# Performance work log

Measured on AMD Instinct MI355X. Metric: run time of the kernel, lower is better.

The kernel has to match this reference:

```python
import jax, jax.numpy as jnp
import numpy as np

TEMP = 0.02
KD_W = 1.0
VSD_W = 1.0
VLAD_W = 1.0
CON_W = 1.0
MSE_W = 1.0

B, SS, ST, DS, DT, V, NV, NT = 8, 96, 128, 1024, 2048, 32000, 32, 64


def hungarian(cost):
    # Shortest-augmenting-path assignment (e-maxx / Jonker-Volgenant style).
    # Square cost [n, n]; returns col_of_row so that row i matches column
    # col_of_row[i] with minimal total cost (same as scipy linear_sum_assignment).
    cost = np.asarray(cost, dtype=np.float64)
    n = cost.shape[0]
    INF = 1e18
    u = np.zeros(n + 1)
    v = np.zeros(n + 1)
    p = np.zeros(n + 1, dtype=np.int64)
    way = np.zeros(n + 1, dtype=np.int64)
    for i in range(1, n + 1):
        p[0] = i
        j0 = 0
        minv = np.full(n + 1, INF)
        used = np.zeros(n + 1, dtype=bool)
        while True:
            used[j0] = True
            i0 = p[j0]
            js = np.nonzero(~used)[0]
            js = js[js > 0]
            cur = cost[i0 - 1, js - 1] - u[i0] - v[js]
            upd = cur < minv[js]
            minv[js] = np.where(upd, cur, minv[js])
            way[js] = np.where(upd, j0, way[js])
            k = int(np.argmin(minv[js]))
            delta = minv[js][k]
            j1 = int(js[k])
            u[p[used]] += delta
            v[used] -= delta
            minv[~used] -= delta
            j0 = j1
            if p[j0] == 0:
                break
        while j0:
            j1 = int(way[j0])
            p[j0] = p[j1]
            j0 = j1
    col_of_row = np.zeros(n, dtype=np.int64)
    for j in range(1, n + 1):
        col_of_row[p[j] - 1] = j - 1
    return col_of_row


def _match(s_logits, t_logits):
    # Per-sample L1 (p=1 cdist) cost between teacher rows and student cols,
    # then Hungarian matching. Host-side loop is unavoidable (sequential
    # combinatorial algorithm), matching the original per-sample scipy loop.
    idx = []
    for b in range(s_logits.shape[0]):
        cost = np.abs(t_logits[b][:, None, :] - s_logits[b][None, :, :]).sum(-1)
        idx.append(hungarian(cost))
    return np.stack(idx)


def _cosine(a, b, eps=1e-8):
    # a: [B, M, D], b: [B, N, D] -> [B, M, N]; torch F.cosine_similarity semantics
    an = a / jnp.maximum(jnp.linalg.norm(a, axis=-1, keepdims=True), eps)
    bn = b / jnp.maximum(jnp.linalg.norm(b, axis=-1, keepdims=True), eps)
    return jnp.einsum('bmd,bnd->bmn', an, bn)


def setup_inputs() -> dict:
    key = jax.random.key(0)
    ks = jax.random.split(key, 12)
    f = jax.random.normal
    return {
        's_qry_reps': f(ks[0], (B, DS), jnp.float32),
        's_pos_reps': f(ks[1], (B, DS), jnp.float32),
        't_qry_reps': f(ks[2], (B, DT), jnp.float32),
        't_pos_reps': f(ks[3], (B, DT), jnp.float32),
        's_hidden_qry': f(ks[4], (B, SS, DS), jnp.float32),
        's_hidden_pos': f(ks[5], (B, SS, DS), jnp.float32),
        't_hidden_qry': f(ks[6], (B, ST, DT), jnp.float32),
        't_hidden_pos': f(ks[7], (B, ST, DT), jnp.float32),
        'W_s_lm': f(ks[8], (DS, V), jnp.float32) / np.float32(np.sqrt(DS)),
        'W_t_lm': f(ks[9], (DT, V), jnp.float32) / np.float32(np.sqrt(DT)),
        'W_proj': f(ks[10], (DT, DS), jnp.float32) / np.float32(np.sqrt(DT)),
        'b_proj': jnp.zeros((DS,), jnp.float32),
        'nv': NV,
        'nt': NT,
    }


def reference(s_qry_reps, s_pos_reps, t_qry_reps, t_pos_reps,
              s_hidden_qry, s_hidden_pos, t_hidden_qry, t_hidden_pos,
              W_s_lm, W_t_lm, W_proj, b_proj, nv, nt):
    Bn = s_qry_reps.shape[0]
    # 1) contrastive InfoNCE (world_size=1 -> gather is identity, target=arange)
    scores = (s_qry_reps @ s_pos_reps.T) / TEMP
    logp = jax.nn.log_softmax(scores, axis=-1)
    contrastive = -jnp.mean(jnp.diagonal(logp))
    # 2) MSE vs t2s-projected teacher reps
    mse = 0.5 * (jnp.mean((s_qry_reps - (t_qry_reps @ W_proj + b_proj)) ** 2)
                 + jnp.mean((s_pos_reps - (t_pos_reps @ W_proj + b_proj)) ** 2))
    # 3/4) VSD + VLAD over qry and pos sides stacked -> [2B, ...]
    s_hid = jnp.concatenate([s_hidden_qry, s_hidden_pos], axis=0)
    t_hid = jnp.concatenate([t_hidden_qry, t_hidden_pos], axis=0)
    St = t_hid.shape[1]
    sv = s_hid[:, :nv]                      # student vision tokens   [2B, Nv, DS]
    st = s_hid[:, nv:nv + nt]               # student text tokens     [2B, Nt, DS]
    tv = t_hid[:, St - nv - nt:St - nt]     # teacher vision tokens   [2B, Nv, DT]
    tt = t_hid[:, St - nt:]                 # teacher text tokens     [2B, Nt, DT]
    s_logits = jnp.einsum('bnd,dv->bnv', sv, W_s_lm)   # [2B, Nv, V]
    t_logits = jnp.einsum('bnd,dv->bnv', tv, W_t_lm)   # [2B, Nv, V]
    # Hungarian matching on detached logits (host side, like the original)
    idx = jnp.asarray(_match(np.asarray(s_logits), np.asarray(t_logits)))  # [2B, Nv]
    # VSD: MSE between matched student logits and teacher logits (t order = arange)
    s_logits_m = jnp.take_along_axis(s_logits, idx[:, :, None], axis=1)
    vsd = jnp.sum(jnp.mean((s_logits_m - t_logits) ** 2, axis=(1, 2)))
    # VLAD: smooth-L1 on vision->text cosine affinity maps
    sv_m = jnp.take_along_axis(sv, idx[:, :, None], axis=1)
    d = _cosine(sv_m, st) - _cosine(tv, tt)            # [2B, Nv, Nt]
    ad = jnp.abs(d)
    sl1 = jnp.where(ad < 1.0, 0.5 * d * d, ad - 0.5)
    vlad = jnp.sum(jnp.mean(sl1, axis=(1, 2)))
    distill = (VSD_W * vsd + VLAD_W * vlad) / Bn
    loss = CON_W * contrastive + MSE_W * mse + KD_W * distill
    return loss, contrastive, distill
```

## Files before the change

### kernel.cpp

```cpp
#include <hip/hip_runtime.h>
#include <math.h>

#define DS_ 1024
#define DT_ 2048
#define V_  32000
#define SS_ 96
#define ST_ 128


__device__ __forceinline__ float block_reduce_sum_256(float v) {
  __shared__ float tmp[4];
  #pragma unroll
  for (int off = 32; off; off >>= 1) v += __shfl_xor(v, off);
  const int wid = threadIdx.x >> 6;
  if ((threadIdx.x & 63) == 0) tmp[wid] = v;
  __syncthreads();
  if (threadIdx.x == 0) v = tmp[0] + tmp[1] + tmp[2] + tmp[3];
  return v;
}

__device__ __forceinline__ const float* s_base(int b, const float* s_hq, const float* s_hp) {
  return (b < 8) ? (s_hq + (size_t)b * SS_ * DS_) : (s_hp + (size_t)(b - 8) * SS_ * DS_);
}
__device__ __forceinline__ const float* t_base(int b, const float* t_hq, const float* t_hp) {
  return (b < 8) ? (t_hq + (size_t)b * ST_ * DT_) : (t_hp + (size_t)(b - 8) * ST_ * DT_);
}

__device__ __forceinline__ unsigned short f2bf(float x) {
  unsigned int u = __float_as_uint(x);
  u += 0x7fffu + ((u >> 16) & 1u);
  return (unsigned short)(u >> 16);
}
__device__ __forceinline__ float bf2f(unsigned short u) {
  return __uint_as_float(((unsigned int)u) << 16);
}

using bf16x8 = __attribute__((ext_vector_type(8))) short;
using f32x4  = __attribute__((ext_vector_type(4))) float;
using u16x4  = __attribute__((ext_vector_type(4))) unsigned short;

__device__ __forceinline__ void gll16(const void* g, void* l) {
  __builtin_amdgcn_global_load_lds((const __attribute__((address_space(1))) unsigned int*)g,
                                   (__attribute__((address_space(3))) unsigned int*)l, 16, 0, 0);
}

__device__ __forceinline__ unsigned int wave_umin_dpp(unsigned int r) {
  unsigned int t;
  t = (unsigned int)__builtin_amdgcn_update_dpp((int)r, (int)r, 0x111, 0xF, 0xF, false); r = r < t ? r : t;
  t = (unsigned int)__builtin_amdgcn_update_dpp((int)r, (int)r, 0x112, 0xF, 0xF, false); r = r < t ? r : t;
  t = (unsigned int)__builtin_amdgcn_update_dpp((int)r, (int)r, 0x114, 0xF, 0xF, false); r = r < t ? r : t;
  t = (unsigned int)__builtin_amdgcn_update_dpp((int)r, (int)r, 0x118, 0xF, 0xF, false); r = r < t ? r : t;
  t = (unsigned int)__builtin_amdgcn_update_dpp((int)r, (int)r, 0x142, 0xF, 0xF, false); r = r < t ? r : t;
  t = (unsigned int)__builtin_amdgcn_update_dpp((int)r, (int)r, 0x143, 0xF, 0xF, false); r = r < t ? r : t;
  return r;
}


__device__ __forceinline__ void scores_body(int blk, const float* __restrict__ sq,
                                            const float* __restrict__ sp,
                                            float* __restrict__ scores) {
  const int i = blk >> 3, j = blk & 7;
  float acc = 0.f;
  for (int k = threadIdx.x; k < DS_; k += 256)
    acc += sq[(size_t)i * DS_ + k] * sp[(size_t)j * DS_ + k];
  acc = block_reduce_sum_256(acc);
  if (threadIdx.x == 0) scores[i * 8 + j] = acc * 50.0f;
}

__device__ __forceinline__ void proj2_body(int kc, const float* __restrict__ t_qry,
                                           const float* __restrict__ t_pos,
                                           const float* __restrict__ Wp,
                                           float* __restrict__ proj,
                                           unsigned char* smem) {
  float (*tv)[64] = (float (*)[64])smem;
  const int tid = threadIdx.x;
  for (int s = tid; s < 16 * 64; s += 256) {
    const int zi = s >> 6, k = s & 63;
    const float* t = (zi >= 8) ? (t_pos + (size_t)(zi - 8) * DT_) : (t_qry + (size_t)zi * DT_);
    tv[zi][k] = t[kc * 64 + k];
  }
  __syncthreads();
  const int d4 = tid * 4;
  float4 acc[16];
  #pragma unroll
  for (int zi = 0; zi < 16; ++zi) acc[zi] = (float4){0.f, 0.f, 0.f, 0.f};
  for (int k = 0; k < 64; ++k) {
    const float4 w = *(const float4*)&Wp[(size_t)(kc * 64 + k) * DS_ + d4];
    #pragma unroll
    for (int zi = 0; zi < 16; ++zi) {
      const float t = tv[zi][k];
      acc[zi].x += t * w.x; acc[zi].y += t * w.y;
      acc[zi].z += t * w.z; acc[zi].w += t * w.w;
    }
  }
  #pragma unroll
  for (int zi = 0; zi < 16; ++zi) {
    float* p = proj + (size_t)zi * DS_ + d4;
    atomicAdd(&p[0], acc[zi].x); atomicAdd(&p[1], acc[zi].y);
    atomicAdd(&p[2], acc[zi].z); atomicAdd(&p[3], acc[zi].w);
  }
}

__device__ __forceinline__ void norms_body(int blk, const float* __restrict__ s_hq,
                                           const float* __restrict__ s_hp,
                                           const float* __restrict__ t_hq,
                                           const float* __restrict__ t_hp,
                                           float* __restrict__ invn) {
  const int b = blk / 192, t = blk % 192;
  const float* bs = s_base(b, s_hq, s_hp);
  const float* bt = t_base(b, t_hq, t_hp);
  const float* row;
  int K;
  float* out;
  if (t < 32)       { row = bs + (size_t)t * DS_;             K = DS_; out = invn + b * 32 + t; }
  else if (t < 96)  { row = bs + (size_t)t * DS_;             K = DS_; out = invn + 512 + b * 64 + (t - 32); }
  else if (t < 128) { row = bt + (size_t)(t - 96 + 32) * DT_;  K = DT_; out = invn + 1536 + b * 32 + (t - 96); }
  else              { row = bt + (size_t)(t - 128 + 64) * DT_; K = DT_; out = invn + 2048 + b * 64 + (t - 128); }
  float ss = 0.f;
  for (int k = threadIdx.x; k < K; k += 256) { const float x = row[k]; ss += x * x; }
  ss = block_reduce_sum_256(ss);
  if (threadIdx.x == 0) *out = 1.0f / fmaxf(sqrtf(ss), 1e-8f);
}

__device__ __forceinline__ void pack_as_body(int g, const float* __restrict__ s_hq,
                                             const float* __restrict__ s_hp,
                                             unsigned short* __restrict__ As) {
  const int b = g >> 5, i = g & 31;
  const float* src = s_base(b, s_hq, s_hp) + (size_t)i * DS_;
  const int k4 = threadIdx.x * 4;
  const float4 w = *(const float4*)&src[k4];
  u16x4 o; o[0] = f2bf(w.x); o[1] = f2bf(w.y); o[2] = f2bf(w.z); o[3] = f2bf(w.w);
  *(u16x4*)&As[(size_t)g * DS_ + k4] = o;
}

__device__ __forceinline__ void pack_at_body(int g, const float* __restrict__ t_hq,
                                             const float* __restrict__ t_hp,
                                             unsigned short* __restrict__ At) {
  const int b = g >> 5, i = g & 31;
  const float* src = t_base(b, t_hq, t_hp) + (size_t)(32 + i) * DT_;
  #pragma unroll
  for (int it = 0; it < 2; ++it) {
    const int k4 = (threadIdx.x + it * 256) * 4;
    const float4 w = *(const float4*)&src[k4];
    u16x4 o; o[0] = f2bf(w.x); o[1] = f2bf(w.y); o[2] = f2bf(w.z); o[3] = f2bf(w.w);
    *(u16x4*)&At[(size_t)g * DT_ + k4] = o;
  }
}

__device__ __forceinline__ void convw_body(int id, const float* __restrict__ W,
                                           unsigned short* __restrict__ Wbt,
                                           int K, unsigned char* smem) {
  float (*tile)[65] = (float (*)[65])smem;
  const int v0 = (id % 500) * 64, k0 = (id / 500) * 64;
  const int tid = threadIdx.x;
  #pragma unroll
  for (int it = 0; it < 4; ++it) {
    const int kr = (tid >> 4) + it * 16;
    const int v4 = (tid & 15) * 4;
    const float4 w = *(const float4*)&W[(size_t)(k0 + kr) * V_ + v0 + v4];
    tile[v4 + 0][kr] = w.x; tile[v4 + 1][kr] = w.y;
    tile[v4 + 2][kr] = w.z; tile[v4 + 3][kr] = w.w;
  }
  __syncthreads();
  #pragma unroll
  for (int it = 0; it < 2; ++it) {
    const int s = tid + it * 256;
    const int v = s >> 3, ch = s & 7;
    const float* src = &tile[v][ch * 8];
    unsigned int o[4];
    #pragma unroll
    for (int q = 0; q < 4; ++q)
      o[q] = (unsigned int)f2bf(src[2 * q]) | ((unsigned int)f2bf(src[2 * q + 1]) << 16);
    uint4 pk = {o[0], o[1], o[2], o[3]};
    *(uint4*)&Wbt[(size_t)(v0 + v) * K + k0 + ch * 8] = pk;
  }
}

__device__ __forceinline__ void dt_body(int id, const float* __restrict__ t_hq,
                                        const float* __restrict__ t_hp,
                                        const float* __restrict__ invn,
                                        float* __restrict__ ct) {
  const int b = id >> 5, i = id & 31;
  const int wv = threadIdx.x >> 6, lane = threadIdx.x & 63;
  const float* bt = t_base(b, t_hq, t_hp);
  const float* a2p = bt + (size_t)(32 + i) * DT_;
  float a2[32];
  #pragma unroll
  for (int q = 0; q < 32; ++q) a2[q] = a2p[lane + 64 * q];
  const float in_t = invn[1536 + b * 32 + i];
  for (int jj = 0; jj < 16; ++jj) {
    const int j = wv * 16 + jj;
    const float* b2 = bt + (size_t)(64 + j) * DT_;
    float dt = 0.f;
    #pragma unroll
    for (int q = 0; q < 32; ++q) dt += a2[q] * b2[lane + 64 * q];
    #pragma unroll
    for (int off = 32; off; off >>= 1) dt += __shfl_xor(dt, off);
    if (lane == 0) ct[(b * 32 + i) * 64 + j] = dt * in_t * invn[2048 + b * 64 + j];
  }
}


template <int K>
__device__ __forceinline__ void gemm_body(int blk, int nwg,
                                          const unsigned short* __restrict__ A,
                                          const unsigned short* __restrict__ Wbt,
                                          unsigned short* __restrict__ Out,
                                          unsigned char* smem) {
  unsigned short* AldsB = (unsigned short*)smem;
  unsigned short* BldsB = (unsigned short*)(smem + 32768);
  const int q = nwg >> 3, r = nwg & 7;
  const int xcd = blk & 7, off = blk >> 3;
  const int sblk = (xcd < r ? xcd * (q + 1) : r * (q + 1) + (xcd - r) * q) + off;
  const int m0 = (sblk & 1) * 256;
  const int n0 = (sblk >> 1) * 128;
  const int tid = threadIdx.x;
  const int wv = tid >> 6, lane = tid & 63;
  const int lr = lane & 15, cc = lane >> 4;

  f32x4 acc[4][8];
  #pragma unroll
  for (int mf = 0; mf < 4; ++mf)
    #pragma unroll
    for (int nf = 0; nf < 8; ++nf) acc[mf][nf] = (f32x4){0.f, 0.f, 0.f, 0.f};

  constexpr int NT = K / 32;

  auto stage = [&](int kt, int buf) {
    #pragma unroll
    for (int it = 0; it < 4; ++it) {
      const int slot = it * 256 + tid;
      const int row = slot >> 2, cs = slot & 3;
      gll16(A + (size_t)(m0 + row) * K + kt * 32 + ((cs ^ ((row >> 1) & 3)) << 3),
            AldsB + (size_t)buf * 8192 + (size_t)(it * 256 + wv * 64) * 8);
    }
    #pragma unroll
    for (int it = 0; it < 2; ++it) {
      const int slot = it * 256 + tid;
      const int row = slot >> 2, cs = slot & 3;
      gll16(Wbt + (size_t)(n0 + row) * K + kt * 32 + ((cs ^ ((row >> 1) & 3)) << 3),
            BldsB + (size_t)buf * 4096 + (size_t)(it * 256 + wv * 64) * 8);
    }
  };

  stage(0, 0);
  if (NT > 1) stage(1, 1);
  for (int kt = 0; kt < NT; ++kt) {
    const int cur = kt & 1;
    if (kt >= 1 && kt + 1 < NT) stage(kt + 1, cur ^ 1);
    if (kt + 1 < NT) asm volatile("s_waitcnt vmcnt(6)" ::: "memory");
    else             asm volatile("s_waitcnt vmcnt(0)" ::: "memory");
    asm volatile("s_barrier" ::: "memory");
    bf16x8 af[4];
    #pragma unroll
    for (int mf = 0; mf < 4; ++mf) {
      const int row = wv * 64 + mf * 16 + lr;
      af[mf] = *(const bf16x8*)(AldsB + cur * 8192 + row * 32 + ((cc ^ ((row >> 1) & 3)) << 3));
    }
    __builtin_amdgcn_s_setprio(1);
    #pragma unroll
    for (int nf = 0; nf < 8; ++nf) {
      const int vr = nf * 16 + lr;
      const bf16x8 bfr = *(const bf16x8*)(BldsB + cur * 4096 + vr * 32 + ((cc ^ ((vr >> 1) & 3)) << 3));
      #pragma unroll
      for (int mf = 0; mf < 4; ++mf)
        acc[mf][nf] = __builtin_amdgcn_mfma_f32_16x16x32_bf16(af[mf], bfr, acc[mf][nf], 0, 0, 0);
    }
    __builtin_amdgcn_s_setprio(0);
    asm volatile("s_barrier" ::: "memory");
  }

  unsigned short* Olds = AldsB;
  #pragma unroll
  for (int h = 0; h < 2; ++h) {
    if (h) __syncthreads();
    #pragma unroll
    for (int mf = 0; mf < 4; ++mf)
      #pragma unroll
      for (int nf4 = 0; nf4 < 4; ++nf4) {
        const int nf = h * 4 + nf4;
        #pragma unroll
        for (int q2 = 0; q2 < 4; ++q2) {
          const int row = wv * 64 + mf * 16 + (lane >> 4) * 4 + q2;
          const int col = nf4 * 16 + lr;
          Olds[row * 64 + (col ^ (((row >> 2) & 3) << 4))] = f2bf(acc[mf][nf][q2]);
        }
      }
    __syncthreads();
    #pragma unroll
    for (int it = 0; it < 4; ++it) {
      const int slot = it * 256 + tid;
      const int row = slot >> 3, c2 = slot & 7;
      const uint4 pk = *(const uint4*)&Olds[row * 64 + ((c2 ^ (((row >> 2) & 3) << 1)) << 3)];
      *(uint4*)&Out[(size_t)(m0 + row) * V_ + n0 + h * 64 + c2 * 8] = pk;
    }
  }
}


__global__ __launch_bounds__(256) void fused_pre_kernel(const float* __restrict__ s_qry,
                                                        const float* __restrict__ s_pos,
                                                        const float* __restrict__ t_qry,
                                                        const float* __restrict__ t_pos,
                                                        const float* __restrict__ s_hq,
                                                        const float* __restrict__ s_hp,
                                                        const float* __restrict__ t_hq,
                                                        const float* __restrict__ t_hp,
                                                        const float* __restrict__ Ws,
                                                        const float* __restrict__ Wp,
                                                        float* __restrict__ scores,
                                                        float* __restrict__ proj,
                                                        float* __restrict__ invn,
                                                        unsigned short* __restrict__ As,
                                                        unsigned short* __restrict__ At,
                                                        unsigned short* __restrict__ Wsb) {
  __shared__ __align__(16) unsigned char smem[16640];
  const int blk = blockIdx.x;
  if (blk < 64)            scores_body(blk, s_qry, s_pos, scores);
  else if (blk < 96)       proj2_body(blk - 64, t_qry, t_pos, Wp, proj, smem);
  else if (blk < 3168)     norms_body(blk - 96, s_hq, s_hp, t_hq, t_hp, invn);
  else if (blk < 3680)     pack_as_body(blk - 3168, s_hq, s_hp, As);
  else if (blk < 4192)     pack_at_body(blk - 3680, t_hq, t_hp, At);
  else                     convw_body(blk - 4192, Ws, Wsb, DS_, smem);
}

__global__ __launch_bounds__(256) void fused_mid_kernel(const unsigned short* __restrict__ As,
                                                        const unsigned short* __restrict__ Wsb,
                                                        unsigned short* __restrict__ Sg,
                                                        const float* __restrict__ Wt,
                                                        unsigned short* __restrict__ Wtb,
                                                        const float* __restrict__ t_hq,
                                                        const float* __restrict__ t_hp,
                                                        const float* __restrict__ invn,
                                                        float* __restrict__ ct) {
  __shared__ __align__(16) unsigned char smem[49152];
  const int blk = blockIdx.x;
  if (blk < 500)            gemm_body<DS_>(blk, 500, As, Wsb, Sg, smem);
  else if (blk < 16500)     convw_body(blk - 500, Wt, Wtb, DT_, smem);
  else                      dt_body(blk - 16500, t_hq, t_hp, invn, ct);
}

__global__ __launch_bounds__(256) void gemm_tn_kernel_t(const unsigned short* __restrict__ A,
                                                        const unsigned short* __restrict__ Wbt,
                                                        unsigned short* __restrict__ Out) {
  __shared__ __align__(16) unsigned char smem[49152];
  gemm_body<DT_>(blockIdx.x, (int)gridDim.x, A, Wbt, Out, smem);
}


__global__ __launch_bounds__(256) void mse2_kernel(const float* __restrict__ s_qry,
                                                   const float* __restrict__ s_pos,
                                                   const float* __restrict__ proj,
                                                   const float* __restrict__ bp,
                                                   float* __restrict__ mse_acc) {
  const int z = blockIdx.x >> 3, i = blockIdx.x & 7;
  const float* s = (z ? s_pos : s_qry) + (size_t)i * DS_;
  const float* p = proj + ((size_t)z * 8 + i) * DS_;
  float ss = 0.f;
  for (int d = threadIdx.x; d < DS_; d += 256) {
    const float diff = s[d] - (p[d] + bp[d]);
    ss += diff * diff;
  }
  ss = block_reduce_sum_256(ss);
  if (threadIdx.x == 0) atomicAdd(mse_acc, ss);
}


#define CPV 500
#define CPP 508

__global__ __launch_bounds__(256) void cost_pairs_kernel(const unsigned short* __restrict__ Sg,
                                                         const unsigned short* __restrict__ Tg,
                                                         float* __restrict__ cost1,
                                                         float* __restrict__ cost2) {
  __shared__ __align__(16) unsigned short Sl[32 * CPP];
  __shared__ __align__(16) unsigned short Tl[32 * CPP];
  const int b = blockIdx.x >> 6, sl = blockIdx.x & 63;
  const int v0 = sl * CPV;
  const int tid = threadIdx.x;

  for (int s = tid; s < 32 * 125; s += 256) {
    const int r = s / 125, c = s % 125;
    *(u16x4*)&Sl[r * CPP + c * 4] = *(const u16x4*)&Sg[(size_t)(b * 32 + r) * V_ + v0 + c * 4];
    *(u16x4*)&Tl[r * CPP + c * 4] = *(const u16x4*)&Tg[(size_t)(b * 32 + r) * V_ + v0 + c * 4];
  }
  __syncthreads();

  const int i = tid >> 3, j4 = (tid & 7) * 4;
  float a1[4] = {0.f, 0.f, 0.f, 0.f}, a2[4] = {0.f, 0.f, 0.f, 0.f};
  for (int v = 0; v < CPV; v += 4) {
    const u16x4 t4 = *(const u16x4*)&Tl[i * CPP + v];
    float tf[4];
    #pragma unroll
    for (int q = 0; q < 4; ++q) tf[q] = bf2f(t4[q]);
    #pragma unroll
    for (int jj = 0; jj < 4; ++jj) {
      const u16x4 s4 = *(const u16x4*)&Sl[(j4 + jj) * CPP + v];
      #pragma unroll
      for (int q = 0; q < 4; ++q) {
        const float d = tf[q] - bf2f(s4[q]);
        a1[jj] += fabsf(d);
        a2[jj] += d * d;
      }
    }
  }
  #pragma unroll
  for (int jj = 0; jj < 4; ++jj) {
    atomicAdd(&cost1[(size_t)b * 1024 + i * 32 + j4 + jj], a1[jj]);
    atomicAdd(&cost2[(size_t)b * 1024 + i * 32 + j4 + jj], a2[jj]);
  }
}


__global__ __launch_bounds__(64) void hungarian_kernel(const float* __restrict__ cost1,
                                                       const float* __restrict__ cost2,
                                                       int* __restrict__ idx,
                                                       float* __restrict__ vsd_acc) {
  const int b = blockIdx.x;
  const int lane = threadIdx.x;
  const float INF = __int_as_float(0x7f800000);
  __shared__ float C[32 * 33];
  __shared__ float u_lds[33];

  for (int s = lane; s < 1024; s += 64) {
    const int r = s >> 5, c = s & 31;
    C[r * 33 + c] = cost1[(size_t)b * 1024 + s];
  }
  if (lane == 0) u_lds[0] = 0.f;
  __syncthreads();

  const bool isj = (lane >= 1 && lane <= 32);
  const int cix = isj ? (lane - 1) : 0;

  if (lane < 32) {
    float m = C[lane * 33];
    for (int j = 1; j < 32; ++j) m = fminf(m, C[lane * 33 + j]);
    u_lds[lane + 1] = m;
  }
  __syncthreads();

  float v = 0.f;
  if (isj) {
    float m = INF;
    for (int i = 0; i < 32; ++i) m = fminf(m, C[i * 33 + cix] - u_lds[i + 1]);
    v = m;
  }

  int p = 0;
  unsigned int assigned = 0;
  for (int i = 1; i <= 32; ++i) {
    const float ui = u_lds[i];
    const bool zero = isj && (p == 0) && ((C[(i - 1) * 33 + cix] - ui) == v);
    const unsigned long long tie = __ballot(zero);
    if (tie) {
      const int j1 = __ffsll(tie) - 1;
      if (lane == j1) p = i;
      assigned |= (1u << (i - 1));
    }
  }

  for (int i = 1; i <= 32; ++i) {
    if (assigned & (1u << (i - 1))) continue;
    if (lane == 0) p = i;
    float minv = INF;
    int way = 0;
    int used = 0;
    int j0 = 0;
    float ui0 = u_lds[i];
    float crow = C[(i - 1) * 33 + cix];
    while (true) {
      if (lane == j0) used = 1;
      float val = INF;
      if (isj && !used) {
        const float cur = crow - ui0 - v;
        if (cur < minv) { minv = cur; way = j0; }
        val = minv;
      }
      const unsigned int rb = wave_umin_dpp(__float_as_uint(val));
      const unsigned int minb = (unsigned int)__builtin_amdgcn_readlane((int)rb, 63);
      const float delta = __uint_as_float(minb);
      const unsigned long long tie = __ballot(__float_as_uint(val) == minb);
      const int j1 = __ffsll(tie) - 1;
      const int i0n = __builtin_amdgcn_readlane(p, j1);
      const float ui0n = u_lds[i0n];
      const int nri = (i0n >= 1 ? i0n : 1) - 1;
      const float cnext = C[nri * 33 + cix];
      if (used) {
        u_lds[p] += delta;
        v -= delta;
      } else {
        minv -= delta;
      }
      j0 = j1;
      if (i0n == 0) break;
      ui0 = ui0n;
      crow = cnext;
    }
    while (j0) {
      const int j1 = __builtin_amdgcn_readlane(way, j0);
      const int pv = __builtin_amdgcn_readlane(p, j1);
      if (lane == j0) p = pv;
      j0 = j1;
    }
  }
  float term = 0.f;
  if (isj) {
    idx[b * 32 + (p - 1)] = lane - 1;
    term = cost2[(size_t)b * 1024 + (p - 1) * 32 + (lane - 1)];
  }
  #pragma unroll
  for (int off = 32; off; off >>= 1) term += __shfl_xor(term, off);
  if (lane == 0) atomicAdd(vsd_acc, term);
}


__global__ __launch_bounds__(256) void vlad_final_kernel(const float* __restrict__ s_hq,
                                                         const float* __restrict__ s_hp,
                                                         const int* __restrict__ idx,
                                                         const float* __restrict__ invn,
                                                         const float* __restrict__ ct,
                                                         float* __restrict__ vlad_acc) {
  const int b = blockIdx.x >> 5, i = blockIdx.x & 31;
  const int wv = threadIdx.x >> 6, lane = threadIdx.x & 63;
  const float* bs = s_base(b, s_hq, s_hp);
  const int is = idx[b * 32 + i];
  const float* a1p = bs + (size_t)is * DS_;
  float a1[16];
  #pragma unroll
  for (int q = 0; q < 16; ++q) a1[q] = a1p[lane + 64 * q];
  const float in_s = invn[b * 32 + is];
  float local = 0.f;
  for (int jj = 0; jj < 16; ++jj) {
    const int j = wv * 16 + jj;
    const float* b1 = bs + (size_t)(32 + j) * DS_;
    float ds = 0.f;
    #pragma unroll
    for (int q = 0; q < 16; ++q) ds += a1[q] * b1[lane + 64 * q];
    #pragma unroll
    for (int off = 32; off; off >>= 1) ds += __shfl_xor(ds, off);
    if (lane == 0) {
      const float cs = ds * in_s * invn[512 + b * 64 + j];
      const float d = cs - ct[(b * 32 + i) * 64 + j];
      const float ad = fabsf(d);
      local += (ad < 1.f) ? 0.5f * d * d : ad - 0.5f;
    }
  }
  if (lane == 0) atomicAdd(vlad_acc, local);
}


__global__ __launch_bounds__(64) void final_kernel(const float* __restrict__ scores,
                                                   const float* __restrict__ accs,
                                                   float* __restrict__ out) {
  const int lane = threadIdx.x;
  float ci = 0.f;
  if (lane < 8) {
    float m = -1e30f;
    for (int j = 0; j < 8; ++j) m = fmaxf(m, scores[lane * 8 + j]);
    float sum = 0.f;
    for (int j = 0; j < 8; ++j) sum += expf(scores[lane * 8 + j] - m);
    const float lse = m + logf(sum);
    ci = scores[lane * 8 + lane] - lse;
  }
  #pragma unroll
  for (int off = 32; off; off >>= 1) ci += __shfl_xor(ci, off);
  if (lane == 0) {
    const float contrastive = -ci / 8.0f;
    const float mse = accs[0] / 16384.0f;
    const float vsd = accs[1] / 1024000.0f;
    const float vlad = accs[2] / 2048.0f;
    const float distill = (vsd + vlad) / 8.0f;
    out[0] = contrastive + mse + distill;
    out[1] = contrastive;
    out[2] = distill;
  }
}


extern "C" void kernel_launch(void* const* d_in, const int* in_sizes, int n_in,
                              void* d_out, int out_size, void* d_ws, size_t ws_size,
                              hipStream_t stream) {
  const float* s_qry = (const float*)d_in[0];
  const float* s_pos = (const float*)d_in[1];
  const float* t_qry = (const float*)d_in[2];
  const float* t_pos = (const float*)d_in[3];
  const float* s_hq  = (const float*)d_in[4];
  const float* s_hp  = (const float*)d_in[5];
  const float* t_hq  = (const float*)d_in[6];
  const float* t_hp  = (const float*)d_in[7];
  const float* Ws    = (const float*)d_in[8];
  const float* Wt    = (const float*)d_in[9];
  const float* Wp    = (const float*)d_in[10];
  const float* bp    = (const float*)d_in[11];

  float* ws     = (float*)d_ws;
  float* scores = ws;
  float* cost1  = ws + 64;
  float* cost2  = ws + 16448;
  float* invn   = ws + 32832;
  float* accs   = ws + 35904;
  float* proj   = ws + 35908;
  int*   idx    = (int*)(ws + 52292);
  float* ct     = ws + 52804;
  const size_t small_bytes = (size_t)52804 * 4;

  const size_t As_off = 524288;
  const size_t At_off = As_off + (size_t)512 * DS_ * 2;
  const size_t Ws_off = At_off + (size_t)512 * DT_ * 2;
  const size_t Wt_off = Ws_off + (size_t)V_ * DS_ * 2;
  const size_t Sg_off = Wt_off + (size_t)V_ * DT_ * 2;
  const size_t Tg_off = Sg_off + (size_t)512 * V_ * 2;
  const size_t req2   = Tg_off + (size_t)512 * V_ * 2;

  hipMemsetAsync(d_ws, 0, small_bytes, stream);

  if (ws_size >= req2) {
    unsigned short* As  = (unsigned short*)((char*)d_ws + As_off);
    unsigned short* At  = (unsigned short*)((char*)d_ws + At_off);
    unsigned short* Wsb = (unsigned short*)((char*)d_ws + Ws_off);
    unsigned short* Wtb = (unsigned short*)((char*)d_ws + Wt_off);
    unsigned short* Sg  = (unsigned short*)((char*)d_ws + Sg_off);
    unsigned short* Tg  = (unsigned short*)((char*)d_ws + Tg_off);

    fused_pre_kernel<<<12192, 256, 0, stream>>>(s_qry, s_pos, t_qry, t_pos,
                                                s_hq, s_hp, t_hq, t_hp,
                                                Ws, Wp, scores, proj, invn, As, At, Wsb);
    mse2_kernel<<<16, 256, 0, stream>>>(s_qry, s_pos, proj, bp, accs + 0);

    fused_mid_kernel<<<17012, 256, 0, stream>>>(As, Wsb, Sg, Wt, Wtb,
                                                t_hq, t_hp, invn, ct);

    gemm_tn_kernel_t<<<(V_ / 128) * 2, 256, 0, stream>>>(At, Wtb, Tg);
    cost_pairs_kernel<<<16 * 64, 256, 0, stream>>>(Sg, Tg, cost1, cost2);

    hungarian_kernel<<<16, 64, 0, stream>>>(cost1, cost2, idx, accs + 1);
    vlad_final_kernel<<<512, 256, 0, stream>>>(s_hq, s_hp, idx, invn, ct, accs + 2);
    final_kernel<<<1, 64, 0, stream>>>(scores, accs, (float*)d_out);
  }
}
```

Before: 463.8 us.

## Fuse teacher GEMM with cost computation and precompute VLAD cosine tables

The teacher logits GEMM now computes the L1/L2 pairwise cost directly from its accumulator tile against student logits staged in shared memory. This removes the Tg round trip to global memory and the separate cost_pairs kernel. All student and teacher vision-text dot products are precomputed in the pre kernel, so the post-Hungarian VLAD step becomes a small gather. The mse2 kernel is folded into the mid kernel, which removes launches. In exchange, the GEMM epilogue carries heavy register arrays and many atomics, and the cost loop repeats LDS reads per thread.

```diff
diff --git a/kernel.cpp b/kernel.cpp
--- a/kernel.cpp
+++ b/kernel.cpp
@@ -38,6 +38,7 @@
 using bf16x8 = __attribute__((ext_vector_type(8))) short;
 using f32x4  = __attribute__((ext_vector_type(4))) float;
 using u16x4  = __attribute__((ext_vector_type(4))) unsigned short;
+using u16x8  = __attribute__((ext_vector_type(8))) unsigned short;
 
 __device__ __forceinline__ void gll16(const void* g, void* l) {
   __builtin_amdgcn_global_load_lds((const __attribute__((address_space(1))) unsigned int*)g,
@@ -178,8 +179,7 @@
 
 __device__ __forceinline__ void dt_body(int id, const float* __restrict__ t_hq,
                                         const float* __restrict__ t_hp,
-                                        const float* __restrict__ invn,
-                                        float* __restrict__ ct) {
+                                        float* __restrict__ dtd) {
   const int b = id >> 5, i = id & 31;
   const int wv = threadIdx.x >> 6, lane = threadIdx.x & 63;
   const float* bt = t_base(b, t_hq, t_hp);
@@ -187,7 +187,6 @@
   float a2[32];
   #pragma unroll
   for (int q = 0; q < 32; ++q) a2[q] = a2p[lane + 64 * q];
-  const float in_t = invn[1536 + b * 32 + i];
   for (int jj = 0; jj < 16; ++jj) {
     const int j = wv * 16 + jj;
     const float* b2 = bt + (size_t)(64 + j) * DT_;
@@ -196,33 +195,60 @@
     for (int q = 0; q < 32; ++q) dt += a2[q] * b2[lane + 64 * q];
     #pragma unroll
     for (int off = 32; off; off >>= 1) dt += __shfl_xor(dt, off);
-    if (lane == 0) ct[(b * 32 + i) * 64 + j] = dt * in_t * invn[2048 + b * 64 + j];
-  }
+    if (lane == 0) dtd[(b * 32 + i) * 64 + j] = dt;
+  }
+}
+
+__device__ __forceinline__ void cs_body(int id, const float* __restrict__ s_hq,
+                                        const float* __restrict__ s_hp,
+                                        float* __restrict__ csd) {
+  const int b = id >> 5, i = id & 31;
+  const int wv = threadIdx.x >> 6, lane = threadIdx.x & 63;
+  const float* bs = s_base(b, s_hq, s_hp);
+  const float* a1p = bs + (size_t)i * DS_;
+  float a1[16];
+  #pragma unroll
+  for (int q = 0; q < 16; ++q) a1[q] = a1p[lane + 64 * q];
+  for (int jj = 0; jj < 16; ++jj) {
+    const int j = wv * 16 + jj;
+    const float* b1 = bs + (size_t)(32 + j) * DS_;
+    float ds = 0.f;
+    #pragma unroll
+    for (int q = 0; q < 16; ++q) ds += a1[q] * b1[lane + 64 * q];
+    #pragma unroll
+    for (int off = 32; off; off >>= 1) ds += __shfl_xor(ds, off);
+    if (lane == 0) csd[(b * 32 + i) * 64 + j] = ds;
+  }
+}
+
+__device__ __forceinline__ void mse2_body(int blk, const float* __restrict__ s_qry,
+                                          const float* __restrict__ s_pos,
+                                          const float* __restrict__ proj,
+                                          const float* __restrict__ bp,
+                                          float* __restrict__ mse_acc) {
+  const int z = blk >> 3, i = blk & 7;
+  const float* s = (z ? s_pos : s_qry) + (size_t)i * DS_;
+  const float* p = proj + ((size_t)z * 8 + i) * DS_;
+  float ss = 0.f;
+  for (int d = threadIdx.x; d < DS_; d += 256) {
+    const float diff = s[d] - (p[d] + bp[d]);
+    ss += diff * diff;
+  }
+  ss = block_reduce_sum_256(ss);
+  if (threadIdx.x == 0) atomicAdd(mse_acc, ss);
 }
 
 
 template <int K>
-__device__ __forceinline__ void gemm_body(int blk, int nwg,
-                                          const unsigned short* __restrict__ A,
-                                          const unsigned short* __restrict__ Wbt,
-                                          unsigned short* __restrict__ Out,
-                                          unsigned char* smem) {
+__device__ __forceinline__ void gemm_mainloop(int m0, int n0,
+                                              const unsigned short* __restrict__ A,
+                                              const unsigned short* __restrict__ Wbt,
+                                              f32x4 (&acc)[4][8], unsigned char* smem) {
   unsigned short* AldsB = (unsigned short*)smem;
   unsigned short* BldsB = (unsigned short*)(smem + 32768);
-  const int q = nwg >> 3, r = nwg & 7;
-  const int xcd = blk & 7, off = blk >> 3;
-  const int sblk = (xcd < r ? xcd * (q + 1) : r * (q + 1) + (xcd - r) * q) + off;
-  const int m0 = (sblk & 1) * 256;
-  const int n0 = (sblk >> 1) * 128;
   const int tid = threadIdx.x;
   const int wv = tid >> 6, lane = tid & 63;
   const int lr = lane & 15, cc = lane >> 4;
-
-  f32x4 acc[4][8];
-  #pragma unroll
-  for (int mf = 0; mf < 4; ++mf)
-    #pragma unroll
-    for (int nf = 0; nf < 8; ++nf) acc[mf][nf] = (f32x4){0.f, 0.f, 0.f, 0.f};
 
   constexpr int NT = K / 32;
 
@@ -269,8 +295,31 @@
     __builtin_amdgcn_s_setprio(0);
     asm volatile("s_barrier" ::: "memory");
   }
-
-  unsigned short* Olds = AldsB;
+}
+
+__device__ __forceinline__ void gemm_store_body(int blk, int nwg,
+                                                const unsigned short* __restrict__ A,
+                                                const unsigned short* __restrict__ Wbt,
+                                                unsigned short* __restrict__ Out,
+                                                unsigned char* smem) {
+  const int q = nwg >> 3, r = nwg & 7;
+  const int xcd = blk & 7, off = blk >> 3;
+  const int sblk = (xcd < r ? xcd * (q + 1) : r * (q + 1) + (xcd - r) * q) + off;
+  const int m0 = (sblk & 1) * 256;
+  const int n0 = (sblk >> 1) * 128;
+  const int tid = threadIdx.x;
+  const int wv = tid >> 6, lane = tid & 63;
+  const int lr = lane & 15;
+
+  f32x4 acc[4][8];
+  #pragma unroll
+  for (int mf = 0; mf < 4; ++mf)
+    #pragma unroll
+    for (int nf = 0; nf < 8; ++nf) acc[mf][nf] = (f32x4){0.f, 0.f, 0.f, 0.f};
+
+  gemm_mainloop<DS_>(m0, n0, A, Wbt, acc, smem);
+
+  unsigned short* Olds = (unsigned short*)smem;
   #pragma unroll
   for (int h = 0; h < 2; ++h) {
     if (h) __syncthreads();
@@ -294,6 +343,90 @@
       const uint4 pk = *(const uint4*)&Olds[row * 64 + ((c2 ^ (((row >> 2) & 3) << 1)) << 3)];
       *(uint4*)&Out[(size_t)(m0 + row) * V_ + n0 + h * 64 + c2 * 8] = pk;
     }
+  }
+}
+
+__global__ __launch_bounds__(256) void gemm_cost_kernel(const unsigned short* __restrict__ A,
+                                                        const unsigned short* __restrict__ Wbt,
+                                                        const unsigned short* __restrict__ Sg,
+                                                        float* __restrict__ cost1,
+                                                        float* __restrict__ cost2) {
+  __shared__ __align__(16) unsigned char smem[51200];
+  const int nwg = (int)gridDim.x;
+  const int q = nwg >> 3, r = nwg & 7;
+  const int xcd = blockIdx.x & 7, off = blockIdx.x >> 3;
+  const int sblk = (xcd < r ? xcd * (q + 1) : r * (q + 1) + (xcd - r) * q) + off;
+  const int m0 = (sblk & 1) * 256;
+  const int n0 = (sblk >> 1) * 128;
+  const int tid = threadIdx.x;
+  const int wv = tid >> 6, lane = tid & 63;
+  const int lr = lane & 15;
+
+  f32x4 acc[4][8];
+  #pragma unroll
+  for (int mf = 0; mf < 4; ++mf)
+    #pragma unroll
+    for (int nf = 0; nf < 8; ++nf) acc[mf][nf] = (f32x4){0.f, 0.f, 0.f, 0.f};
+
+  gemm_mainloop<DT_>(m0, n0, A, Wbt, acc, smem);
+
+  unsigned short* Tl   = (unsigned short*)smem;
+  unsigned short* Slds = (unsigned short*)(smem + 34816);
+  const int b8 = tid >> 5;
+  const int i  = tid & 31;
+  float l1[32], l2[32];
+  #pragma unroll
+  for (int j = 0; j < 32; ++j) { l1[j] = 0.f; l2[j] = 0.f; }
+
+  #pragma unroll
+  for (int h = 0; h < 2; ++h) {
+    if (h) __syncthreads();
+    #pragma unroll
+    for (int mf = 0; mf < 4; ++mf)
+      #pragma unroll
+      for (int nf4 = 0; nf4 < 4; ++nf4) {
+        #pragma unroll
+        for (int q2 = 0; q2 < 4; ++q2) {
+          const int row = wv * 64 + mf * 16 + (lane >> 4) * 4 + q2;
+          const int col = nf4 * 16 + lr;
+          Tl[row * 68 + col] = f2bf(acc[mf][h * 4 + nf4][q2]);
+        }
+      }
+    #pragma unroll
+    for (int qq = 0; qq < 2; ++qq) {
+      __syncthreads();
+      const int vbase = n0 + h * 64 + qq * 32;
+      #pragma unroll
+      for (int it = 0; it < 4; ++it) {
+        const int slot = it * 256 + tid;
+        const int srow = slot >> 2, c16 = slot & 3;
+        *(u16x8*)&Slds[srow * 32 + c16 * 8] =
+            *(const u16x8*)&Sg[(size_t)(m0 + srow) * V_ + vbase + c16 * 8];
+      }
+      __syncthreads();
+      for (int vq = 0; vq < 8; ++vq) {
+        const u16x4 t4 = *(const u16x4*)&Tl[tid * 68 + qq * 32 + vq * 4];
+        float tf[4];
+        #pragma unroll
+        for (int e = 0; e < 4; ++e) tf[e] = bf2f(t4[e]);
+        #pragma unroll
+        for (int j = 0; j < 32; ++j) {
+          const u16x4 s4 = *(const u16x4*)&Slds[(b8 * 32 + j) * 32 + vq * 4];
+          #pragma unroll
+          for (int e = 0; e < 4; ++e) {
+            const float d = tf[e] - bf2f(s4[e]);
+            l1[j] += fabsf(d);
+            l2[j] += d * d;
+          }
+        }
+      }
+    }
+  }
+  const int bglob = (m0 >> 5) + b8;
+  #pragma unroll
+  for (int j = 0; j < 32; ++j) {
+    atomicAdd(&cost1[(size_t)bglob * 1024 + i * 32 + j], l1[j]);
+    atomicAdd(&cost2[(size_t)bglob * 1024 + i * 32 + j], l2[j]);
   }
 }
 
@@ -313,7 +446,9 @@
                                                         float* __restrict__ invn,
                                                         unsigned short* __restrict__ As,
                                                         unsigned short* __restrict__ At,
-                                                        unsigned short* __restrict__ Wsb) {
+                                                        unsigned short* __restrict__ Wsb,
+                                                        float* __restrict__ csd,
+                                                        float* __restrict__ dtd) {
   __shared__ __align__(16) unsigned char smem[16640];
   const int blk = blockIdx.x;
   if (blk < 64)            scores_body(blk, s_qry, s_pos, scores);
@@ -321,7 +456,9 @@
   else if (blk < 3168)     norms_body(blk - 96, s_hq, s_hp, t_hq, t_hp, invn);
   else if (blk < 3680)     pack_as_body(blk - 3168, s_hq, s_hp, As);
   else if (blk < 4192)     pack_at_body(blk - 3680, t_hq, t_hp, At);
-  else                     convw_body(blk - 4192, Ws, Wsb, DS_, smem);
+  else if (blk < 12192)    convw_body(blk - 4192, Ws, Wsb, DS_, smem);
+  else if (blk < 12704)    cs_body(blk - 12192, s_hq, s_hp, csd);
+  else                     dt_body(blk - 12704, t_hq, t_hp, dtd);
 }
 
 __global__ __launch_bounds__(256) void fused_mid_kernel(const unsigned short* __restrict__ As,
@@ -329,86 +466,16 @@
                                                         unsigned short* __restrict__ Sg,
                                                         const float* __restrict__ Wt,
                                                         unsigned short* __restrict__ Wtb,
-                                                        const float* __restrict__ t_hq,
-                                                        const float* __restrict__ t_hp,
-                                                        const float* __restrict__ invn,
-                                                        float* __restrict__ ct) {
+                                                        const float* __restrict__ s_qry,
+                                                        const float* __restrict__ s_pos,
+                                                        const float* __restrict__ proj,
+                                                        const float* __restrict__ bp,
+                                                        float* __restrict__ mse_acc) {
   __shared__ __align__(16) unsigned char smem[49152];
   const int blk = blockIdx.x;
-  if (blk < 500)            gemm_body<DS_>(blk, 500, As, Wsb, Sg, smem);
+  if (blk < 500)            gemm_store_body(blk, 500, As, Wsb, Sg, smem);
   else if (blk < 16500)     convw_body(blk - 500, Wt, Wtb, DT_, smem);
-  else                      dt_body(blk - 16500, t_hq, t_hp, invn, ct);
-}
-
-__global__ __launch_bounds__(256) void gemm_tn_kernel_t(const unsigned short* __restrict__ A,
-                                                        const unsigned short* __restrict__ Wbt,
-                                                        unsigned short* __restrict__ Out) {
-  __shared__ __align__(16) unsigned char smem[49152];
-  gemm_body<DT_>(blockIdx.x, (int)gridDim.x, A, Wbt, Out, smem);
-}
-
-
-__global__ __launch_bounds__(256) void mse2_kernel(const float* __restrict__ s_qry,
-                                                   const float* __restrict__ s_pos,
-                                                   const float* __restrict__ proj,
-                                                   const float* __restrict__ bp,
-                                                   float* __restrict__ mse_acc) {
-  const int z = blockIdx.x >> 3, i = blockIdx.x & 7;
-  const float* s = (z ? s_pos : s_qry) + (size_t)i * DS_;
-  const float* p = proj + ((size_t)z * 8 + i) * DS_;
-  float ss = 0.f;
-  for (int d = threadIdx.x; d < DS_; d += 256) {
-    const float diff = s[d] - (p[d] + bp[d]);
-    ss += diff * diff;
-  }
-  ss = block_reduce_sum_256(ss);
-  if (threadIdx.x == 0) atomicAdd(mse_acc, ss);
-}
-
-
-#define CPV 500
-#define CPP 508
-
-__global__ __launch_bounds__(256) void cost_pairs_kernel(const unsigned short* __restrict__ Sg,
-                                                         const unsigned short* __restrict__ Tg,
-                                                         float* __restrict__ cost1,
-                                                         float* __restrict__ cost2) {
-  __shared__ __align__(16) unsigned short Sl[32 * CPP];
-  __shared__ __align__(16) unsigned short Tl[32 * CPP];
-  const int b = blockIdx.x >> 6, sl = blockIdx.x & 63;
-  const int v0 = sl * CPV;
-  const int tid = threadIdx.x;
-
-  for (int s = tid; s < 32 * 125; s += 256) {
-    const int r = s / 125, c = s % 125;
-    *(u16x4*)&Sl[r * CPP + c * 4] = *(const u16x4*)&Sg[(size_t)(b * 32 + r) * V_ + v0 + c * 4];
-    *(u16x4*)&Tl[r * CPP + c * 4] = *(const u16x4*)&Tg[(size_t)(b * 32 + r) * V_ + v0 + c * 4];
-  }
-  __syncthreads();
-
-  const int i = tid >> 3, j4 = (tid & 7) * 4;
-  float a1[4] = {0.f, 0.f, 0.f, 0.f}, a2[4] = {0.f, 0.f, 0.f, 0.f};
-  for (int v = 0; v < CPV; v += 4) {
-    const u16x4 t4 = *(const u16x4*)&Tl[i * CPP + v];
-    float tf[4];
-    #pragma unroll
-    for (int q = 0; q < 4; ++q) tf[q] = bf2f(t4[q]);
-    #pragma unroll
-    for (int jj = 0; jj < 4; ++jj) {
-      const u16x4 s4 = *(const u16x4*)&Sl[(j4 + jj) * CPP + v];
-      #pragma unroll
-      for (int q = 0; q < 4; ++q) {
-        const float d = tf[q] - bf2f(s4[q]);
-        a1[jj] += fabsf(d);
-        a2[jj] += d * d;
-      }
-    }
-  }
-  #pragma unroll
-  for (int jj = 0; jj < 4; ++jj) {
-    atomicAdd(&cost1[(size_t)b * 1024 + i * 32 + j4 + jj], a1[jj]);
-    atomicAdd(&cost2[(size_t)b * 1024 + i * 32 + j4 + jj], a2[jj]);
-  }
+  else                      mse2_body(blk - 16500, s_qry, s_pos, proj, bp, mse_acc);
 }
 
 
@@ -514,38 +581,26 @@
 }
 
 
-__global__ __launch_bounds__(256) void vlad_final_kernel(const float* __restrict__ s_hq,
-                                                         const float* __restrict__ s_hp,
-                                                         const int* __restrict__ idx,
-                                                         const float* __restrict__ invn,
-                                                         const float* __restrict__ ct,
-                                                         float* __restrict__ vlad_acc) {
-  const int b = blockIdx.x >> 5, i = blockIdx.x & 31;
-  const int wv = threadIdx.x >> 6, lane = threadIdx.x & 63;
-  const float* bs = s_base(b, s_hq, s_hp);
-  const int is = idx[b * 32 + i];
-  const float* a1p = bs + (size_t)is * DS_;
-  float a1[16];
-  #pragma unroll
-  for (int q = 0; q < 16; ++q) a1[q] = a1p[lane + 64 * q];
-  const float in_s = invn[b * 32 + is];
+__global__ __launch_bounds__(256) void vlad_gather_kernel(const int* __restrict__ idx,
+                                                          const float* __restrict__ invn,
+                                                          const float* __restrict__ csd,
+                                                          const float* __restrict__ dtd,
+                                                          float* __restrict__ vlad_acc) {
+  const int b = blockIdx.x;
   float local = 0.f;
-  for (int jj = 0; jj < 16; ++jj) {
-    const int j = wv * 16 + jj;
-    const float* b1 = bs + (size_t)(32 + j) * DS_;
-    float ds = 0.f;
-    #pragma unroll
-    for (int q = 0; q < 16; ++q) ds += a1[q] * b1[lane + 64 * q];
-    #pragma unroll
-    for (int off = 32; off; off >>= 1) ds += __shfl_xor(ds, off);
-    if (lane == 0) {
-      const float cs = ds * in_s * invn[512 + b * 64 + j];
-      const float d = cs - ct[(b * 32 + i) * 64 + j];
-      const float ad = fabsf(d);
-      local += (ad < 1.f) ? 0.5f * d * d : ad - 0.5f;
-    }
-  }
-  if (lane == 0) atomicAdd(vlad_acc, local);
+  #pragma unroll
+  for (int w = 0; w < 8; ++w) {
+    const int cell = threadIdx.x * 8 + w;
+    const int i = cell >> 6, j = cell & 63;
+    const int is = idx[b * 32 + i];
+    const float cs = csd[(b * 32 + is) * 64 + j] * invn[b * 32 + is] * invn[512 + b * 64 + j];
+    const float ct = dtd[(b * 32 + i) * 64 + j] * invn[1536 + b * 32 + i] * invn[2048 + b * 64 + j];
+    const float d = cs - ct;
+    const float ad = fabsf(d);
+    local += (ad < 1.f) ? 0.5f * d * d : ad - 0.5f;
+  }
+  local = block_reduce_sum_256(local);
+  if (threadIdx.x == 0) atomicAdd(vlad_acc, local);
 }
 
 
@@ -601,7 +656,8 @@
   float* accs   = ws + 35904;
   float* proj   = ws + 35908;
   int*   idx    = (int*)(ws + 52292);
-  float* ct     = ws + 52804;
+  float* csd    = ws + 52804;
+  float* dtd    = ws + 85572;
   const size_t small_bytes = (size_t)52804 * 4;
 
   const size_t As_off = 524288;
@@ -609,8 +665,7 @@
   const size_t Ws_off = At_off + (size_t)512 * DT_ * 2;
   const size_t Wt_off = Ws_off + (size_t)V_ * DS_ * 2;
   const size_t Sg_off = Wt_off + (size_t)V_ * DT_ * 2;
-  const size_t Tg_off = Sg_off + (size_t)512 * V_ * 2;
-  const size_t req2   = Tg_off + (size_t)512 * V_ * 2;
+  const size_t req2   = Sg_off + (size_t)512 * V_ * 2;
 
   hipMemsetAsync(d_ws, 0, small_bytes, stream);
 
@@ -620,21 +675,19 @@
     unsigned short* Wsb = (unsigned short*)((char*)d_ws + Ws_off);
     unsigned short* Wtb = (unsigned short*)((char*)d_ws + Wt_off);
     unsigned short* Sg  = (unsigned short*)((char*)d_ws + Sg_off);
-    unsigned short* Tg  = (unsigned short*)((char*)d_ws + Tg_off);
-
-    fused_pre_kernel<<<12192, 256, 0, stream>>>(s_qry, s_pos, t_qry, t_pos,
+
+    fused_pre_kernel<<<13216, 256, 0, stream>>>(s_qry, s_pos, t_qry, t_pos,
                                                 s_hq, s_hp, t_hq, t_hp,
-                                                Ws, Wp, scores, proj, invn, As, At, Wsb);
-    mse2_kernel<<<16, 256, 0, stream>>>(s_qry, s_pos, proj, bp, accs + 0);
-
-    fused_mid_kernel<<<17012, 256, 0, stream>>>(As, Wsb, Sg, Wt, Wtb,
-                                                t_hq, t_hp, invn, ct);
-
-    gemm_tn_kernel_t<<<(V_ / 128) * 2, 256, 0, stream>>>(At, Wtb, Tg);
-    cost_pairs_kernel<<<16 * 64, 256, 0, stream>>>(Sg, Tg, cost1, cost2);
+                                                Ws, Wp, scores, proj, invn,
+                                                As, At, Wsb, csd, dtd);
+
+    fused_mid_kernel<<<16516, 256, 0, stream>>>(As, Wsb, Sg, Wt, Wtb,
+                                                s_qry, s_pos, proj, bp, accs + 0);
+
+    gemm_cost_kernel<<<(V_ / 128) * 2, 256, 0, stream>>>(At, Wtb, Sg, cost1, cost2);
 
     hungarian_kernel<<<16, 64, 0, stream>>>(cost1, cost2, idx, accs + 1);
-    vlad_final_kernel<<<512, 256, 0, stream>>>(s_hq, s_hp, idx, invn, ct, accs + 2);
+    vlad_gather_kernel<<<16, 256, 0, stream>>>(idx, invn, csd, dtd, accs + 2);
     final_kernel<<<1, 64, 0, stream>>>(scores, accs, (float*)d_out);
   }
 }
```

Result: slower. 828.5 us (+78.6%).

## Precompute student/teacher dot-product maps early and gather after matching

Applied to the files above, without the earlier changes.

The student vision·text dot products are now computed for all rows before matching, alongside the teacher ones, inside the first fused kernel. After the Hungarian step, a small gather kernel permutes the precomputed rows and applies the norms and smooth-L1. The aim is to take the 512-block dot-product kernel off the critical path behind the serial Hungarian step. The MSE kernel is also folded into the mid fused kernel to save a launch. The cost is a larger first kernel and an extra workspace buffer.

```diff
diff --git a/kernel.cpp b/kernel.cpp
--- a/kernel.cpp
+++ b/kernel.cpp
@@ -178,8 +178,7 @@
 
 __device__ __forceinline__ void dt_body(int id, const float* __restrict__ t_hq,
                                         const float* __restrict__ t_hp,
-                                        const float* __restrict__ invn,
-                                        float* __restrict__ ct) {
+                                        float* __restrict__ dtd) {
   const int b = id >> 5, i = id & 31;
   const int wv = threadIdx.x >> 6, lane = threadIdx.x & 63;
   const float* bt = t_base(b, t_hq, t_hp);
@@ -187,7 +186,6 @@
   float a2[32];
   #pragma unroll
   for (int q = 0; q < 32; ++q) a2[q] = a2p[lane + 64 * q];
-  const float in_t = invn[1536 + b * 32 + i];
   for (int jj = 0; jj < 16; ++jj) {
     const int j = wv * 16 + jj;
     const float* b2 = bt + (size_t)(64 + j) * DT_;
@@ -196,8 +194,47 @@
     for (int q = 0; q < 32; ++q) dt += a2[q] * b2[lane + 64 * q];
     #pragma unroll
     for (int off = 32; off; off >>= 1) dt += __shfl_xor(dt, off);
-    if (lane == 0) ct[(b * 32 + i) * 64 + j] = dt * in_t * invn[2048 + b * 64 + j];
-  }
+    if (lane == 0) dtd[(b * 32 + i) * 64 + j] = dt;
+  }
+}
+
+__device__ __forceinline__ void cs_body(int id, const float* __restrict__ s_hq,
+                                        const float* __restrict__ s_hp,
+                                        float* __restrict__ csd) {
+  const int b = id >> 5, i = id & 31;
+  const int wv = threadIdx.x >> 6, lane = threadIdx.x & 63;
+  const float* bs = s_base(b, s_hq, s_hp);
+  const float* a1p = bs + (size_t)i * DS_;
+  float a1[16];
+  #pragma unroll
+  for (int q = 0; q < 16; ++q) a1[q] = a1p[lane + 64 * q];
+  for (int jj = 0; jj < 16; ++jj) {
+    const int j = wv * 16 + jj;
+    const float* b1 = bs + (size_t)(32 + j) * DS_;
+    float ds = 0.f;
+    #pragma unroll
+    for (int q = 0; q < 16; ++q) ds += a1[q] * b1[lane + 64 * q];
+    #pragma unroll
+    for (int off = 32; off; off >>= 1) ds += __shfl_xor(ds, off);
+    if (lane == 0) csd[(b * 32 + i) * 64 + j] = ds;
+  }
+}
+
+__device__ __forceinline__ void mse2_body(int blk, const float* __restrict__ s_qry,
+                                          const float* __restrict__ s_pos,
+                                          const float* __restrict__ proj,
+                                          const float* __restrict__ bp,
+                                          float* __restrict__ mse_acc) {
+  const int z = blk >> 3, i = blk & 7;
+  const float* s = (z ? s_pos : s_qry) + (size_t)i * DS_;
+  const float* p = proj + ((size_t)z * 8 + i) * DS_;
+  float ss = 0.f;
+  for (int d = threadIdx.x; d < DS_; d += 256) {
+    const float diff = s[d] - (p[d] + bp[d]);
+    ss += diff * diff;
+  }
+  ss = block_reduce_sum_256(ss);
+  if (threadIdx.x == 0) atomicAdd(mse_acc, ss);
 }
 
 
@@ -313,7 +350,9 @@
                                                         float* __restrict__ invn,
                                                         unsigned short* __restrict__ As,
                                                         unsigned short* __restrict__ At,
-                                                        unsigned short* __restrict__ Wsb) {
+                                                        unsigned short* __restrict__ Wsb,
+                                                        float* __restrict__ csd,
+                                                        float* __restrict__ dtd) {
   __shared__ __align__(16) unsigned char smem[16640];
   const int blk = blockIdx.x;
   if (blk < 64)            scores_body(blk, s_qry, s_pos, scores);
@@ -321,7 +360,9 @@
   else if (blk < 3168)     norms_body(blk - 96, s_hq, s_hp, t_hq, t_hp, invn);
   else if (blk < 3680)     pack_as_body(blk - 3168, s_hq, s_hp, As);
   else if (blk < 4192)     pack_at_body(blk - 3680, t_hq, t_hp, At);
-  else                     convw_body(blk - 4192, Ws, Wsb, DS_, smem);
+  else if (blk < 12192)    convw_body(blk - 4192, Ws, Wsb, DS_, smem);
+  else if (blk < 12704)    cs_body(blk - 12192, s_hq, s_hp, csd);
+  else                     dt_body(blk - 12704, t_hq, t_hp, dtd);
 }
 
 __global__ __launch_bounds__(256) void fused_mid_kernel(const unsigned short* __restrict__ As,
@@ -329,15 +370,16 @@
                                                         unsigned short* __restrict__ Sg,
                                                         const float* __restrict__ Wt,
                                                         unsigned short* __restrict__ Wtb,
-                                                        const float* __restrict__ t_hq,
-                                                        const float* __restrict__ t_hp,
-                                                        const float* __restrict__ invn,
-                                                        float* __restrict__ ct) {
+                                                        const float* __restrict__ s_qry,
+                                                        const float* __restrict__ s_pos,
+                                                        const float* __restrict__ proj,
+                                                        const float* __restrict__ bp,
+                                                        float* __restrict__ mse_acc) {
   __shared__ __align__(16) unsigned char smem[49152];
   const int blk = blockIdx.x;
   if (blk < 500)            gemm_body<DS_>(blk, 500, As, Wsb, Sg, smem);
   else if (blk < 16500)     convw_body(blk - 500, Wt, Wtb, DT_, smem);
-  else                      dt_body(blk - 16500, t_hq, t_hp, invn, ct);
+  else                      mse2_body(blk - 16500, s_qry, s_pos, proj, bp, mse_acc);
 }
 
 __global__ __launch_bounds__(256) void gemm_tn_kernel_t(const unsigned short* __restrict__ A,
@@ -345,24 +387,6 @@
                                                         unsigned short* __restrict__ Out) {
   __shared__ __align__(16) unsigned char smem[49152];
   gemm_body<DT_>(blockIdx.x, (int)gridDim.x, A, Wbt, Out, smem);
-}
-
-
-__global__ __launch_bounds__(256) void mse2_kernel(const float* __restrict__ s_qry,
-                                                   const float* __restrict__ s_pos,
-                                                   const float* __restrict__ proj,
-                                                   const float* __restrict__ bp,
-                                                   float* __restrict__ mse_acc) {
-  const int z = blockIdx.x >> 3, i = blockIdx.x & 7;
-  const float* s = (z ? s_pos : s_qry) + (size_t)i * DS_;
-  const float* p = proj + ((size_t)z * 8 + i) * DS_;
-  float ss = 0.f;
-  for (int d = threadIdx.x; d < DS_; d += 256) {
-    const float diff = s[d] - (p[d] + bp[d]);
-    ss += diff * diff;
-  }
-  ss = block_reduce_sum_256(ss);
-  if (threadIdx.x == 0) atomicAdd(mse_acc, ss);
 }
 
 
@@ -514,38 +538,26 @@
 }
 
 
-__global__ __launch_bounds__(256) void vlad_final_kernel(const float* __restrict__ s_hq,
-                                                         const float* __restrict__ s_hp,
-                                                         const int* __restrict__ idx,
-                                                         const float* __restrict__ invn,
-                                                         const float* __restrict__ ct,
-                                                         float* __restrict__ vlad_acc) {
-  const int b = blockIdx.x >> 5, i = blockIdx.x & 31;
-  const int wv = threadIdx.x >> 6, lane = threadIdx.x & 63;
-  const float* bs = s_base(b, s_hq, s_hp);
-  const int is = idx[b * 32 + i];
-  const float* a1p = bs + (size_t)is * DS_;
-  float a1[16];
-  #pragma unroll
-  for (int q = 0; q < 16; ++q) a1[q] = a1p[lane + 64 * q];
-  const float in_s = invn[b * 32 + is];
+__global__ __launch_bounds__(256) void vlad_gather_kernel(const int* __restrict__ idx,
+                                                          const float* __restrict__ invn,
+                                                          const float* __restrict__ csd,
+                                                          const float* __restrict__ dtd,
+                                                          float* __restrict__ vlad_acc) {
+  const int b = blockIdx.x;
   float local = 0.f;
-  for (int jj = 0; jj < 16; ++jj) {
-    const int j = wv * 16 + jj;
-    const float* b1 = bs + (size_t)(32 + j) * DS_;
-    float ds = 0.f;
-    #pragma unroll
-    for (int q = 0; q < 16; ++q) ds += a1[q] * b1[lane + 64 * q];
-    #pragma unroll
-    for (int off = 32; off; off >>= 1) ds += __shfl_xor(ds, off);
-    if (lane == 0) {
-      const float cs = ds * in_s * invn[512 + b * 64 + j];
-      const float d = cs - ct[(b * 32 + i) * 64 + j];
-      const float ad = fabsf(d);
-      local += (ad < 1.f) ? 0.5f * d * d : ad - 0.5f;
-    }
-  }
-  if (lane == 0) atomicAdd(vlad_acc, local);
+  #pragma unroll
+  for (int w = 0; w < 8; ++w) {
+    const int cell = threadIdx.x * 8 + w;
+    const int i = cell >> 6, j = cell & 63;
+    const int is = idx[b * 32 + i];
+    const float cs = csd[(b * 32 + is) * 64 + j] * invn[b * 32 + is] * invn[512 + b * 64 + j];
+    const float ct = dtd[(b * 32 + i) * 64 + j] * invn[1536 + b * 32 + i] * invn[2048 + b * 64 + j];
+    const float d = cs - ct;
+    const float ad = fabsf(d);
+    local += (ad < 1.f) ? 0.5f * d * d : ad - 0.5f;
+  }
+  local = block_reduce_sum_256(local);
+  if (threadIdx.x == 0) atomicAdd(vlad_acc, local);
 }
 
 
@@ -601,7 +613,8 @@
   float* accs   = ws + 35904;
   float* proj   = ws + 35908;
   int*   idx    = (int*)(ws + 52292);
-  float* ct     = ws + 52804;
+  float* csd    = ws + 52804;
+  float* dtd    = ws + 85572;
   const size_t small_bytes = (size_t)52804 * 4;
 
   const size_t As_off = 524288;
@@ -622,19 +635,19 @@
     unsigned short* Sg  = (unsigned short*)((char*)d_ws + Sg_off);
     unsigned short* Tg  = (unsigned short*)((char*)d_ws + Tg_off);
 
-    fused_pre_kernel<<<12192, 256, 0, stream>>>(s_qry, s_pos, t_qry, t_pos,
+    fused_pre_kernel<<<13216, 256, 0, stream>>>(s_qry, s_pos, t_qry, t_pos,
                                                 s_hq, s_hp, t_hq, t_hp,
-                                                Ws, Wp, scores, proj, invn, As, At, Wsb);
-    mse2_kernel<<<16, 256, 0, stream>>>(s_qry, s_pos, proj, bp, accs + 0);
-
-    fused_mid_kernel<<<17012, 256, 0, stream>>>(As, Wsb, Sg, Wt, Wtb,
-                                                t_hq, t_hp, invn, ct);
+                                                Ws, Wp, scores, proj, invn,
+                                                As, At, Wsb, csd, dtd);
+
+    fused_mid_kernel<<<16516, 256, 0, stream>>>(As, Wsb, Sg, Wt, Wtb,
+                                                s_qry, s_pos, proj, bp, accs + 0);
 
     gemm_tn_kernel_t<<<(V_ / 128) * 2, 256, 0, stream>>>(At, Wtb, Tg);
     cost_pairs_kernel<<<16 * 64, 256, 0, stream>>>(Sg, Tg, cost1, cost2);
 
     hungarian_kernel<<<16, 64, 0, stream>>>(cost1, cost2, idx, accs + 1);
-    vlad_final_kernel<<<512, 256, 0, stream>>>(s_hq, s_hp, idx, invn, ct, accs + 2);
+    vlad_gather_kernel<<<16, 256, 0, stream>>>(idx, invn, csd, dtd, accs + 2);
     final_kernel<<<1, 64, 0, stream>>>(scores, accs, (float*)d_out);
   }
 }
```

Result: faster. 429.1 us (median of 2 runs) (-7.5%).
